# Kernel optimization log

Hardware: AMD Instinct MI355X
Metric: run time of the kernel (lower is better)

Reference implementation:

```python
import jax, jax.numpy as jnp
import numpy as np
from jax import lax

ENC_DIM, DEC_DIM, ATT_DIM, CONV_CH, KSIZE, ATT_ODIM = 1024, 1024, 512, 32, 50, 1024
SCALING = 2.0


def setup_inputs() -> dict:
    key = jax.random.key(0)
    ks = jax.random.split(key, 12)
    B, T = 32, 2000
    enc_pad = jax.random.normal(ks[0], (B, T, ENC_DIM), dtype=jnp.float32)
    enc_len = jax.random.randint(ks[1], (B,), 1000, T + 1, dtype=jnp.int32)
    dec_h = jax.random.normal(ks[2], (B, 1, DEC_DIM), dtype=jnp.float32)
    att_prev = jax.random.uniform(ks[3], (B, T), dtype=jnp.float32)
    s = 0.02
    W_enc = jax.random.normal(ks[4], (ENC_DIM, ATT_DIM), dtype=jnp.float32) * s
    b_enc = jnp.zeros((ATT_DIM,), jnp.float32)
    W_dec = jax.random.normal(ks[5], (DEC_DIM, ATT_DIM), dtype=jnp.float32) * s
    b_dec = jnp.zeros((ATT_DIM,), jnp.float32)
    W_att = jax.random.normal(ks[6], (CONV_CH, ATT_DIM), dtype=jnp.float32) * s
    b_att = jnp.zeros((ATT_DIM,), jnp.float32)
    # Conv2d(1, C, kernel=(1, 2K+1)) acting on (B,1,1,T) == 1D conv kernel (C,1,2K+1)
    conv_w = jax.random.normal(ks[7], (CONV_CH, 1, 2 * KSIZE + 1), dtype=jnp.float32) * s
    gvec = jax.random.normal(ks[8], (ATT_DIM, 1), dtype=jnp.float32) * s
    W_o = jax.random.normal(ks[9], (ENC_DIM, ATT_ODIM), dtype=jnp.float32) * s
    b_o = jnp.zeros((ATT_ODIM,), jnp.float32)
    return {"enc_pad": enc_pad, "enc_len": enc_len, "dec_h": dec_h, "att_prev": att_prev,
            "W_enc": W_enc, "b_enc": b_enc, "W_dec": W_dec, "b_dec": b_dec,
            "W_att": W_att, "b_att": b_att, "conv_w": conv_w, "gvec": gvec,
            "W_o": W_o, "b_o": b_o}


def reference(enc_pad, enc_len, dec_h, att_prev, W_enc, b_enc, W_dec, b_dec,
              W_att, b_att, conv_w, gvec, W_o, b_o):
    B, T, _ = enc_pad.shape
    enc_h = enc_pad @ W_enc + b_enc                           # [B,T,A]
    # location conv: (B,1,T) * (C,1,K) -> (B,C,T), SAME padding
    att_conv = lax.conv_general_dilated(
        att_prev[:, None, :], conv_w, window_strides=(1,),
        padding=[(KSIZE, KSIZE)], dimension_numbers=("NCH", "OIH", "NCH"))
    att_conv = jnp.transpose(att_conv, (0, 2, 1)) @ W_att + b_att  # [B,T,A]
    dec_term = (dec_h.reshape(B, DEC_DIM) @ W_dec + b_dec)[:, None, :]  # [B,1,A]
    att_state = jnp.tanh(enc_h + dec_term + att_conv)         # [B,T,A]
    e = (att_state @ gvec)[:, :, 0]                           # [B,T]
    mask = jnp.arange(T)[None, :] >= enc_len[:, None]         # True = padded
    e = jnp.where(mask, jnp.float32(-1e15), e)
    attn = jax.nn.softmax(SCALING * e, axis=1)                # [B,T]
    c = jnp.einsum("bt,btd->bd", attn, enc_pad)               # [B,enc_dim]
    c = c @ W_o + b_o                                         # [B,att_odim]
    return c, attn
```

## Files before the change

kernel.cpp:

```cpp
#include <hip/hip_runtime.h>
#include <stdint.h>
#include <stddef.h>

#define T_LEN   2000
#define BATCH   32
#define ROWS    64000
#define KDIM    1024
#define ADIM    512
#define CCH     32
#define KW      101
#define PADA    40

typedef _Float16 half8_t  __attribute__((ext_vector_type(8)));
typedef float    float4_t __attribute__((ext_vector_type(4)));

__device__ __forceinline__ half8_t pack8(float4_t a, float4_t b) {
    half8_t r;
    r[0] = (_Float16)a.x; r[1] = (_Float16)a.y;
    r[2] = (_Float16)a.z; r[3] = (_Float16)a.w;
    r[4] = (_Float16)b.x; r[5] = (_Float16)b.y;
    r[6] = (_Float16)b.z; r[7] = (_Float16)b.w;
    return r;
}

__device__ __forceinline__ float tanh_fast(float x) {
    float ax = __builtin_fabsf(x);
    ax = fminf(ax, 15.f);
    float e = __expf(2.f * ax);
    float t = 1.f - 2.f / (e + 1.f);
    return (x < 0.f) ? -t : t;
}

__device__ __forceinline__ void glds16(const void* g, void* l) {
    __builtin_amdgcn_global_load_lds((const __attribute__((address_space(1))) uint32_t*)g,
                                     (__attribute__((address_space(3))) uint32_t*)l,
                                     16, 0, 0);
}

#define OFF_WENCT 0
#define OFF_WATTT 1048576
#define OFF_CONVA 1081344
#define OFF_DTERM 5177344
#define OFF_EPART 5242880
#define OFF_CPART 5498880

__global__ __launch_bounds__(256) void k_prep_we(const float* __restrict__ We,
                                                 _Float16* __restrict__ Wet) {
    __shared__ float tile[32][33];
    const int k0 = blockIdx.x * 32, n0 = blockIdx.y * 32;
    const int tx = threadIdx.x & 31, ty = threadIdx.x >> 5;
#pragma unroll
    for (int i = 0; i < 4; ++i)
        tile[ty + i * 8][tx] = We[(size_t)(k0 + ty + i * 8) * ADIM + n0 + tx];
    __syncthreads();
#pragma unroll
    for (int i = 0; i < 4; ++i)
        Wet[(size_t)(n0 + ty + i * 8) * KDIM + k0 + tx] = (_Float16)tile[tx][ty + i * 8];
}

__global__ __launch_bounds__(512) void k_prep_wat(const float* __restrict__ Wa,
                                                  _Float16* __restrict__ Wat) {
    const int n = threadIdx.x;
#pragma unroll
    for (int c = 0; c < CCH; ++c)
        Wat[n * CCH + c] = (_Float16)Wa[c * ADIM + n];
}

__global__ __launch_bounds__(256) void k_dterm(const float* __restrict__ dec_h,
                                               const float* __restrict__ W_dec,
                                               const float* __restrict__ be,
                                               const float* __restrict__ bd,
                                               const float* __restrict__ ba,
                                               float* __restrict__ dterm) {
    __shared__ float dh[KDIM];
    __shared__ float part[256];
    const int b = blockIdx.x, a0 = blockIdx.y * 128, tid = threadIdx.x;
#pragma unroll
    for (int i = 0; i < 4; ++i) dh[tid + i * 256] = dec_h[b * KDIM + tid + i * 256];
    __syncthreads();
    const int a = a0 + (tid & 127), kh = (tid >> 7) * 512;
    float s = 0.f;
#pragma unroll 8
    for (int k = 0; k < 512; ++k) s += dh[kh + k] * W_dec[(size_t)(kh + k) * ADIM + a];
    part[tid] = s;
    __syncthreads();
    if (tid < 128) {
        const int aa = a0 + tid;
        dterm[b * ADIM + aa] = part[tid] + part[tid + 128] + be[aa] + bd[aa] + ba[aa];
    }
}

__global__ __launch_bounds__(256) void k_conv(const float* __restrict__ att_prev,
                                              const float* __restrict__ conv_w,
                                              _Float16* __restrict__ convA) {
    __shared__ float ap[128 + 100];
    __shared__ float w[CCH * KW];
    int b = blockIdx.y, tt = blockIdx.x;
    int t0 = tt * 128;
    for (int i = threadIdx.x; i < 228; i += 256) {
        int t = t0 - 50 + i;
        ap[i] = (t >= 0 && t < T_LEN) ? att_prev[b * T_LEN + t] : 0.f;
    }
    for (int i = threadIdx.x; i < CCH * KW; i += 256) w[i] = conv_w[i];
    __syncthreads();
    for (int idx = threadIdx.x; idx < 128 * CCH; idx += 256) {
        int tl = idx >> 5, c = idx & 31;
        int t = t0 + tl;
        if (t < T_LEN) {
            float s = 0.f;
#pragma unroll
            for (int j = 0; j < KW; ++j) s += ap[tl + j] * w[c * KW + j];
            convA[(size_t)(b * T_LEN + t) * CCH + c] = (_Float16)s;
        }
    }
}

__global__ __launch_bounds__(512, 1) void k_gemm_e(const float* __restrict__ enc,
                                                   const _Float16* __restrict__ Wet,
                                                   const _Float16* __restrict__ convA,
                                                   const _Float16* __restrict__ Wat,
                                                   const float* __restrict__ dterm,
                                                   const float* __restrict__ gvec,
                                                   float* __restrict__ epart) {
    __shared__ __attribute__((aligned(16))) _Float16 Ah[128 * PADA];
    __shared__ __attribute__((aligned(16))) _Float16 Bh[512 * 32];

    const int tid  = threadIdx.x;
    const int m0   = blockIdx.x * 128;
    const int wave = tid >> 6, lane = tid & 63;
    const int quad = lane >> 4, c16 = lane & 15;
    const int wm = (wave >> 2) * 64, wn = (wave & 3) * 128;

    float4_t acc[4][8];
#pragma unroll
    for (int i = 0; i < 4; ++i)
#pragma unroll
        for (int j = 0; j < 8; ++j) acc[i][j] = (float4_t){0.f, 0.f, 0.f, 0.f};

    const int arow = tid >> 2, aseg = tid & 3;
    const float* aBase = enc + (size_t)(m0 + arow) * KDIM + aseg * 8;
    const int bl4 = lane >> 2, bseg = lane & 3;

    float4_t pa0 = ((const float4_t*)aBase)[0];
    float4_t pa1 = ((const float4_t*)aBase)[1];

    for (int kk = 0; kk < 32; ++kk) {
        const int k0 = kk * 32;
        __syncthreads();
        *(half8_t*)&Ah[arow * PADA + aseg * 8] = pack8(pa0, pa1);
#pragma unroll
        for (int p = 0; p < 4; ++p) {
            const int nb = wave * 64 + p * 16 + bl4;
            glds16(Wet + (size_t)nb * KDIM + k0 + bseg * 8, &Bh[nb * 32 + bseg * 8]);
        }
        __syncthreads();
        {
            const int kn = (kk < 31) ? (k0 + 32) : k0;
            pa0 = ((const float4_t*)(aBase + kn))[0];
            pa1 = ((const float4_t*)(aBase + kn))[1];
        }
        half8_t af[4], bf[8];
#pragma unroll
        for (int i = 0; i < 4; ++i)
            af[i] = *(const half8_t*)&Ah[(wm + i * 16 + c16) * PADA + quad * 8];
#pragma unroll
        for (int j = 0; j < 8; ++j)
            bf[j] = *(const half8_t*)&Bh[(wn + j * 16 + c16) * 32 + quad * 8];
#pragma unroll
        for (int i = 0; i < 4; ++i)
#pragma unroll
            for (int j = 0; j < 8; ++j)
                acc[i][j] = __builtin_amdgcn_mfma_f32_16x16x32_f16(af[i], bf[j], acc[i][j], 0, 0, 0);
    }

    __syncthreads();
    *(half8_t*)&Ah[arow * PADA + aseg * 8] =
        *(const half8_t*)(convA + (size_t)(m0 + arow) * CCH + aseg * 8);
    {
        const half8_t* bs = (const half8_t*)(Wat + tid * CCH);
#pragma unroll
        for (int s4 = 0; s4 < 4; ++s4) *(half8_t*)&Bh[tid * 32 + s4 * 8] = bs[s4];
    }
    __syncthreads();
    {
        half8_t af[4], bf[8];
#pragma unroll
        for (int i = 0; i < 4; ++i)
            af[i] = *(const half8_t*)&Ah[(wm + i * 16 + c16) * PADA + quad * 8];
#pragma unroll
        for (int j = 0; j < 8; ++j)
            bf[j] = *(const half8_t*)&Bh[(wn + j * 16 + c16) * 32 + quad * 8];
#pragma unroll
        for (int i = 0; i < 4; ++i)
#pragma unroll
            for (int j = 0; j < 8; ++j)
                acc[i][j] = __builtin_amdgcn_mfma_f32_16x16x32_f16(af[i], bf[j], acc[i][j], 0, 0, 0);
    }

    __syncthreads();
    float* e_lds = (float*)Ah;
#pragma unroll
    for (int i = 0; i < 4; ++i) {
        const int rl0 = wm + i * 16 + quad * 4;
#pragma unroll
        for (int r = 0; r < 4; ++r) {
            const int grow = m0 + rl0 + r;
            const int b = grow / T_LEN;
            float s = 0.f;
#pragma unroll
            for (int j = 0; j < 8; ++j) {
                const int col = wn + j * 16 + c16;
                const float v = acc[i][j][r] + dterm[b * ADIM + col];
                s += tanh_fast(v) * gvec[col];
            }
#pragma unroll
            for (int off = 1; off < 16; off <<= 1) s += __shfl_xor(s, off);
            if (c16 == 0) e_lds[(rl0 + r) * 4 + (wave & 3)] = s;
        }
    }
    __syncthreads();
    if (tid < 128) {
        float4_t q = ((const float4_t*)e_lds)[tid];
        epart[m0 + tid] = q.x + q.y + q.z + q.w;
    }
}

__global__ __launch_bounds__(512) void k_softmax(const float* __restrict__ epart,
                                                 const int* __restrict__ enc_len,
                                                 float* __restrict__ attn) {
    __shared__ float ex[T_LEN];
    __shared__ float red[8];
    const int b = blockIdx.x, tid = threadIdx.x;
    const int len = enc_len[b];
    float lmax = -3.4e38f;
    for (int t = tid; t < T_LEN; t += 512) {
        float lg = (t < len) ? 2.f * epart[b * T_LEN + t] : -2e15f;
        ex[t] = lg;
        lmax = fmaxf(lmax, lg);
    }
    for (int off = 1; off < 64; off <<= 1) lmax = fmaxf(lmax, __shfl_xor(lmax, off));
    if ((tid & 63) == 0) red[tid >> 6] = lmax;
    __syncthreads();
    const float m = fmaxf(fmaxf(fmaxf(red[0], red[1]), fmaxf(red[2], red[3])),
                          fmaxf(fmaxf(red[4], red[5]), fmaxf(red[6], red[7])));
    float lsum = 0.f;
    for (int t = tid; t < T_LEN; t += 512) {
        float p = __expf(ex[t] - m);
        ex[t] = p;
        lsum += p;
    }
    for (int off = 1; off < 64; off <<= 1) lsum += __shfl_xor(lsum, off);
    __syncthreads();
    if ((tid & 63) == 0) red[tid >> 6] = lsum;
    __syncthreads();
    const float inv = 1.f / (red[0] + red[1] + red[2] + red[3] + red[4] + red[5] + red[6] + red[7]);
    for (int t = tid; t < T_LEN; t += 512) attn[b * T_LEN + t] = ex[t] * inv;
}

__global__ __launch_bounds__(256) void k_cpart(const float* __restrict__ attn,
                                               const float* __restrict__ enc,
                                               float* __restrict__ cpart) {
    const int b = blockIdx.y, tc = blockIdx.x, tid = threadIdx.x;
    const int t0 = tc * 125;
    float4_t s = (float4_t){0.f, 0.f, 0.f, 0.f};
    const float4_t* ep = (const float4_t*)(enc + (size_t)b * T_LEN * KDIM) + tid;
    const float* ap = attn + b * T_LEN + t0;
#pragma unroll 5
    for (int tt = 0; tt < 125; ++tt) {
        const float w = ap[tt];
        float4_t v = ep[(size_t)(t0 + tt) * 256];
        s += v * w;
    }
    *(float4_t*)&cpart[(size_t)(tc * BATCH + b) * KDIM + tid * 4] = s;
}

__global__ __launch_bounds__(256) void k_out(const float* __restrict__ cpart,
                                             const float* __restrict__ W_o,
                                             const float* __restrict__ b_o,
                                             float* __restrict__ out_c) {
    __shared__ float cm[KDIM];
    const int b = blockIdx.x, tid = threadIdx.x;
    for (int d = tid; d < KDIM; d += 256) {
        float s = 0.f;
#pragma unroll
        for (int p = 0; p < 16; ++p) s += cpart[(size_t)(p * BATCH + b) * KDIM + d];
        cm[d] = s;
    }
    __syncthreads();
    const int o = blockIdx.y * 256 + tid;
    float s = b_o[o];
#pragma unroll 8
    for (int d = 0; d < KDIM; ++d) s += cm[d] * W_o[(size_t)d * KDIM + o];
    out_c[b * KDIM + o] = s;
}

extern "C" void kernel_launch(void* const* d_in, const int* in_sizes, int n_in,
                              void* d_out, int out_size, void* d_ws, size_t ws_size,
                              hipStream_t stream) {
    const float* enc      = (const float*)d_in[0];
    const int*   enc_len  = (const int*)d_in[1];
    const float* dec_h    = (const float*)d_in[2];
    const float* att_prev = (const float*)d_in[3];
    const float* W_enc    = (const float*)d_in[4];
    const float* b_enc    = (const float*)d_in[5];
    const float* W_dec    = (const float*)d_in[6];
    const float* b_dec    = (const float*)d_in[7];
    const float* W_att    = (const float*)d_in[8];
    const float* b_att    = (const float*)d_in[9];
    const float* conv_w   = (const float*)d_in[10];
    const float* gvec     = (const float*)d_in[11];
    const float* W_o      = (const float*)d_in[12];
    const float* b_o      = (const float*)d_in[13];

    float* out_c    = (float*)d_out;
    float* out_attn = out_c + BATCH * KDIM;

    char* ws = (char*)d_ws;
    _Float16* Wet   = (_Float16*)(ws + OFF_WENCT);
    _Float16* Wat   = (_Float16*)(ws + OFF_WATTT);
    _Float16* convA = (_Float16*)(ws + OFF_CONVA);
    float*    dterm = (float*)(ws + OFF_DTERM);
    float*    epart = (float*)(ws + OFF_EPART);
    float*    cpart = (float*)(ws + OFF_CPART);

    k_prep_we<<<dim3(32, 16), 256, 0, stream>>>(W_enc, Wet);
    k_prep_wat<<<1, 512, 0, stream>>>(W_att, Wat);
    k_dterm<<<dim3(BATCH, 4), 256, 0, stream>>>(dec_h, W_dec, b_enc, b_dec, b_att, dterm);
    k_conv<<<dim3(16, BATCH), 256, 0, stream>>>(att_prev, conv_w, convA);
    k_gemm_e<<<500, 512, 0, stream>>>(enc, Wet, convA, Wat, dterm, gvec, epart);
    k_softmax<<<BATCH, 512, 0, stream>>>(epart, enc_len, out_attn);
    k_cpart<<<dim3(16, BATCH), 256, 0, stream>>>(out_attn, enc, cpart);
    k_out<<<dim3(BATCH, 4), 256, 0, stream>>>(cpart, W_o, b_o, out_c);
}
```

Baseline: 628.0 us.

## Merge prep kernels, halve GEMM tile rows, swizzle B LDS, hoist epilogue loads

Four preparation kernels are merged into one launch that dispatches on block index, removing three launches. The main GEMM now uses 64-row tiles with 256 threads and 1000 blocks, so occupancy and CU coverage go up but the same B tile is reloaded twice as often. B rows in LDS get an XOR swizzle to cut bank conflicts. The epilogue hoists gvec and dterm into registers, since a 64-row tile can span at most two batches, and tanh uses a hardware reciprocal.

```diff
diff --git a/kernel.cpp b/kernel.cpp
--- a/kernel.cpp
+++ b/kernel.cpp
@@ -27,7 +27,7 @@
     float ax = __builtin_fabsf(x);
     ax = fminf(ax, 15.f);
     float e = __expf(2.f * ax);
-    float t = 1.f - 2.f / (e + 1.f);
+    float t = 1.f - 2.f * __builtin_amdgcn_rcpf(e + 1.f);
     return (x < 0.f) ? -t : t;
 }
 
@@ -44,92 +44,97 @@
 #define OFF_EPART 5242880
 #define OFF_CPART 5498880
 
-__global__ __launch_bounds__(256) void k_prep_we(const float* __restrict__ We,
-                                                 _Float16* __restrict__ Wet) {
-    __shared__ float tile[32][33];
-    const int k0 = blockIdx.x * 32, n0 = blockIdx.y * 32;
-    const int tx = threadIdx.x & 31, ty = threadIdx.x >> 5;
-#pragma unroll
-    for (int i = 0; i < 4; ++i)
-        tile[ty + i * 8][tx] = We[(size_t)(k0 + ty + i * 8) * ADIM + n0 + tx];
-    __syncthreads();
-#pragma unroll
-    for (int i = 0; i < 4; ++i)
-        Wet[(size_t)(n0 + ty + i * 8) * KDIM + k0 + tx] = (_Float16)tile[tx][ty + i * 8];
-}
-
-__global__ __launch_bounds__(512) void k_prep_wat(const float* __restrict__ Wa,
-                                                  _Float16* __restrict__ Wat) {
-    const int n = threadIdx.x;
-#pragma unroll
-    for (int c = 0; c < CCH; ++c)
-        Wat[n * CCH + c] = (_Float16)Wa[c * ADIM + n];
-}
-
-__global__ __launch_bounds__(256) void k_dterm(const float* __restrict__ dec_h,
-                                               const float* __restrict__ W_dec,
-                                               const float* __restrict__ be,
-                                               const float* __restrict__ bd,
-                                               const float* __restrict__ ba,
-                                               float* __restrict__ dterm) {
-    __shared__ float dh[KDIM];
-    __shared__ float part[256];
-    const int b = blockIdx.x, a0 = blockIdx.y * 128, tid = threadIdx.x;
-#pragma unroll
-    for (int i = 0; i < 4; ++i) dh[tid + i * 256] = dec_h[b * KDIM + tid + i * 256];
-    __syncthreads();
-    const int a = a0 + (tid & 127), kh = (tid >> 7) * 512;
-    float s = 0.f;
+__global__ __launch_bounds__(256) void k_prep(const float* __restrict__ We,
+                                              const float* __restrict__ Wa,
+                                              const float* __restrict__ dec_h,
+                                              const float* __restrict__ W_dec,
+                                              const float* __restrict__ be,
+                                              const float* __restrict__ bd,
+                                              const float* __restrict__ ba,
+                                              const float* __restrict__ att_prev,
+                                              const float* __restrict__ conv_w,
+                                              _Float16* __restrict__ Wet,
+                                              _Float16* __restrict__ Wat,
+                                              float* __restrict__ dterm,
+                                              _Float16* __restrict__ convA) {
+    __shared__ float smem[3460];
+    const int blk = blockIdx.x, tid = threadIdx.x;
+
+    if (blk < 512) {
+        float (*tile)[33] = (float(*)[33])smem;
+        const int k0 = (blk >> 4) * 32, n0 = (blk & 15) * 32;
+        const int tx = tid & 31, ty = tid >> 5;
+#pragma unroll
+        for (int i = 0; i < 4; ++i)
+            tile[ty + i * 8][tx] = We[(size_t)(k0 + ty + i * 8) * ADIM + n0 + tx];
+        __syncthreads();
+#pragma unroll
+        for (int i = 0; i < 4; ++i)
+            Wet[(size_t)(n0 + ty + i * 8) * KDIM + k0 + tx] = (_Float16)tile[tx][ty + i * 8];
+    } else if (blk < 640) {
+        float* dh = smem;
+        float* part = smem + 1024;
+        const int idx = blk - 512, b = idx >> 2, a0 = (idx & 3) * 128;
+#pragma unroll
+        for (int i = 0; i < 4; ++i) dh[tid + i * 256] = dec_h[b * KDIM + tid + i * 256];
+        __syncthreads();
+        const int a = a0 + (tid & 127), kh = (tid >> 7) * 512;
+        float s = 0.f;
 #pragma unroll 8
-    for (int k = 0; k < 512; ++k) s += dh[kh + k] * W_dec[(size_t)(kh + k) * ADIM + a];
-    part[tid] = s;
-    __syncthreads();
-    if (tid < 128) {
-        const int aa = a0 + tid;
-        dterm[b * ADIM + aa] = part[tid] + part[tid + 128] + be[aa] + bd[aa] + ba[aa];
-    }
-}
-
-__global__ __launch_bounds__(256) void k_conv(const float* __restrict__ att_prev,
-                                              const float* __restrict__ conv_w,
-                                              _Float16* __restrict__ convA) {
-    __shared__ float ap[128 + 100];
-    __shared__ float w[CCH * KW];
-    int b = blockIdx.y, tt = blockIdx.x;
-    int t0 = tt * 128;
-    for (int i = threadIdx.x; i < 228; i += 256) {
-        int t = t0 - 50 + i;
-        ap[i] = (t >= 0 && t < T_LEN) ? att_prev[b * T_LEN + t] : 0.f;
-    }
-    for (int i = threadIdx.x; i < CCH * KW; i += 256) w[i] = conv_w[i];
-    __syncthreads();
-    for (int idx = threadIdx.x; idx < 128 * CCH; idx += 256) {
-        int tl = idx >> 5, c = idx & 31;
-        int t = t0 + tl;
-        if (t < T_LEN) {
-            float s = 0.f;
-#pragma unroll
-            for (int j = 0; j < KW; ++j) s += ap[tl + j] * w[c * KW + j];
-            convA[(size_t)(b * T_LEN + t) * CCH + c] = (_Float16)s;
-        }
-    }
-}
-
-__global__ __launch_bounds__(512, 1) void k_gemm_e(const float* __restrict__ enc,
-                                                   const _Float16* __restrict__ Wet,
-                                                   const _Float16* __restrict__ convA,
-                                                   const _Float16* __restrict__ Wat,
-                                                   const float* __restrict__ dterm,
-                                                   const float* __restrict__ gvec,
-                                                   float* __restrict__ epart) {
-    __shared__ __attribute__((aligned(16))) _Float16 Ah[128 * PADA];
+        for (int k = 0; k < 512; ++k) s += dh[kh + k] * W_dec[(size_t)(kh + k) * ADIM + a];
+        part[tid] = s;
+        __syncthreads();
+        if (tid < 128) {
+            const int aa = a0 + tid;
+            dterm[b * ADIM + aa] = part[tid] + part[tid + 128] + be[aa] + bd[aa] + ba[aa];
+        }
+    } else if (blk < 1152) {
+        float* ap = smem;
+        float* w  = smem + 228;
+        const int idx = blk - 640, b = idx >> 4, tt = idx & 15;
+        const int t0 = tt * 128;
+        for (int i = tid; i < 228; i += 256) {
+            int t = t0 - 50 + i;
+            ap[i] = (t >= 0 && t < T_LEN) ? att_prev[b * T_LEN + t] : 0.f;
+        }
+        for (int i = tid; i < CCH * KW; i += 256) w[i] = conv_w[i];
+        __syncthreads();
+        for (int idx2 = tid; idx2 < 128 * CCH; idx2 += 256) {
+            int tl = idx2 >> 5, c = idx2 & 31;
+            int t = t0 + tl;
+            if (t < T_LEN) {
+                float s = 0.f;
+#pragma unroll
+                for (int j = 0; j < KW; ++j) s += ap[tl + j] * w[c * KW + j];
+                convA[(size_t)(b * T_LEN + t) * CCH + c] = (_Float16)s;
+            }
+        }
+    } else {
+#pragma unroll
+        for (int rr = 0; rr < 2; ++rr) {
+            const int n = tid * 2 + rr;
+#pragma unroll
+            for (int c = 0; c < CCH; ++c)
+                Wat[n * CCH + c] = (_Float16)Wa[c * ADIM + n];
+        }
+    }
+}
+
+__global__ __launch_bounds__(256) void k_gemm_e(const float* __restrict__ enc,
+                                                const _Float16* __restrict__ Wet,
+                                                const _Float16* __restrict__ convA,
+                                                const _Float16* __restrict__ Wat,
+                                                const float* __restrict__ dterm,
+                                                const float* __restrict__ gvec,
+                                                float* __restrict__ epart) {
+    __shared__ __attribute__((aligned(16))) _Float16 Ah[64 * PADA];
     __shared__ __attribute__((aligned(16))) _Float16 Bh[512 * 32];
 
     const int tid  = threadIdx.x;
-    const int m0   = blockIdx.x * 128;
+    const int m0   = blockIdx.x * 64;
     const int wave = tid >> 6, lane = tid & 63;
     const int quad = lane >> 4, c16 = lane & 15;
-    const int wm = (wave >> 2) * 64, wn = (wave & 3) * 128;
+    const int wn = wave * 128;
 
     float4_t acc[4][8];
 #pragma unroll
@@ -139,7 +144,7 @@
 
     const int arow = tid >> 2, aseg = tid & 3;
     const float* aBase = enc + (size_t)(m0 + arow) * KDIM + aseg * 8;
-    const int bl4 = lane >> 2, bseg = lane & 3;
+    const int rowl = lane >> 2, segst = lane & 3;
 
     float4_t pa0 = ((const float4_t*)aBase)[0];
     float4_t pa1 = ((const float4_t*)aBase)[1];
@@ -149,9 +154,10 @@
         __syncthreads();
         *(half8_t*)&Ah[arow * PADA + aseg * 8] = pack8(pa0, pa1);
 #pragma unroll
-        for (int p = 0; p < 4; ++p) {
-            const int nb = wave * 64 + p * 16 + bl4;
-            glds16(Wet + (size_t)nb * KDIM + k0 + bseg * 8, &Bh[nb * 32 + bseg * 8]);
+        for (int p = 0; p < 8; ++p) {
+            const int nb = wn + p * 16 + rowl;
+            const int segsrc = segst ^ ((nb >> 1) & 3);
+            glds16(Wet + (size_t)nb * KDIM + k0 + segsrc * 8, &Bh[(wn + p * 16) * 32]);
         }
         __syncthreads();
         {
@@ -162,10 +168,13 @@
         half8_t af[4], bf[8];
 #pragma unroll
         for (int i = 0; i < 4; ++i)
-            af[i] = *(const half8_t*)&Ah[(wm + i * 16 + c16) * PADA + quad * 8];
-#pragma unroll
-        for (int j = 0; j < 8; ++j)
-            bf[j] = *(const half8_t*)&Bh[(wn + j * 16 + c16) * 32 + quad * 8];
+            af[i] = *(const half8_t*)&Ah[(i * 16 + c16) * PADA + quad * 8];
+#pragma unroll
+        for (int j = 0; j < 8; ++j) {
+            const int r = wn + j * 16 + c16;
+            const int sb = quad ^ ((r >> 1) & 3);
+            bf[j] = *(const half8_t*)&Bh[r * 32 + sb * 8];
+        }
 #pragma unroll
         for (int i = 0; i < 4; ++i)
 #pragma unroll
@@ -176,20 +185,26 @@
     __syncthreads();
     *(half8_t*)&Ah[arow * PADA + aseg * 8] =
         *(const half8_t*)(convA + (size_t)(m0 + arow) * CCH + aseg * 8);
-    {
-        const half8_t* bs = (const half8_t*)(Wat + tid * CCH);
-#pragma unroll
-        for (int s4 = 0; s4 < 4; ++s4) *(half8_t*)&Bh[tid * 32 + s4 * 8] = bs[s4];
+#pragma unroll
+    for (int rr = 0; rr < 2; ++rr) {
+        const int n = tid * 2 + rr;
+        const int sw = (n >> 1) & 3;
+#pragma unroll
+        for (int s = 0; s < 4; ++s)
+            *(half8_t*)&Bh[n * 32 + s * 8] = *(const half8_t*)(Wat + n * CCH + (s ^ sw) * 8);
     }
     __syncthreads();
     {
         half8_t af[4], bf[8];
 #pragma unroll
         for (int i = 0; i < 4; ++i)
-            af[i] = *(const half8_t*)&Ah[(wm + i * 16 + c16) * PADA + quad * 8];
-#pragma unroll
-        for (int j = 0; j < 8; ++j)
-            bf[j] = *(const half8_t*)&Bh[(wn + j * 16 + c16) * 32 + quad * 8];
+            af[i] = *(const half8_t*)&Ah[(i * 16 + c16) * PADA + quad * 8];
+#pragma unroll
+        for (int j = 0; j < 8; ++j) {
+            const int r = wn + j * 16 + c16;
+            const int sb = quad ^ ((r >> 1) & 3);
+            bf[j] = *(const half8_t*)&Bh[r * 32 + sb * 8];
+        }
 #pragma unroll
         for (int i = 0; i < 4; ++i)
 #pragma unroll
@@ -197,29 +212,37 @@
                 acc[i][j] = __builtin_amdgcn_mfma_f32_16x16x32_f16(af[i], bf[j], acc[i][j], 0, 0, 0);
     }
 
+    float g[8], dt0[8], dt1[8];
+    const int b0 = m0 / T_LEN, bt = (m0 + 63) / T_LEN;
+    const int lim = (b0 + 1) * T_LEN;
+#pragma unroll
+    for (int j = 0; j < 8; ++j) {
+        const int col = wn + j * 16 + c16;
+        g[j]   = gvec[col];
+        dt0[j] = dterm[b0 * ADIM + col];
+        dt1[j] = dterm[bt * ADIM + col];
+    }
     __syncthreads();
     float* e_lds = (float*)Ah;
 #pragma unroll
     for (int i = 0; i < 4; ++i) {
-        const int rl0 = wm + i * 16 + quad * 4;
 #pragma unroll
         for (int r = 0; r < 4; ++r) {
-            const int grow = m0 + rl0 + r;
-            const int b = grow / T_LEN;
+            const int rl = i * 16 + quad * 4 + r;
+            const bool hi = (m0 + rl) >= lim;
             float s = 0.f;
 #pragma unroll
             for (int j = 0; j < 8; ++j) {
-                const int col = wn + j * 16 + c16;
-                const float v = acc[i][j][r] + dterm[b * ADIM + col];
-                s += tanh_fast(v) * gvec[col];
+                const float dv = hi ? dt1[j] : dt0[j];
+                s += tanh_fast(acc[i][j][r] + dv) * g[j];
             }
 #pragma unroll
             for (int off = 1; off < 16; off <<= 1) s += __shfl_xor(s, off);
-            if (c16 == 0) e_lds[(rl0 + r) * 4 + (wave & 3)] = s;
-        }
-    }
-    __syncthreads();
-    if (tid < 128) {
+            if (c16 == 0) e_lds[rl * 4 + wave] = s;
+        }
+    }
+    __syncthreads();
+    if (tid < 64) {
         float4_t q = ((const float4_t*)e_lds)[tid];
         epart[m0 + tid] = q.x + q.y + q.z + q.w;
     }
@@ -323,11 +346,9 @@
     float*    epart = (float*)(ws + OFF_EPART);
     float*    cpart = (float*)(ws + OFF_CPART);
 
-    k_prep_we<<<dim3(32, 16), 256, 0, stream>>>(W_enc, Wet);
-    k_prep_wat<<<1, 512, 0, stream>>>(W_att, Wat);
-    k_dterm<<<dim3(BATCH, 4), 256, 0, stream>>>(dec_h, W_dec, b_enc, b_dec, b_att, dterm);
-    k_conv<<<dim3(16, BATCH), 256, 0, stream>>>(att_prev, conv_w, convA);
-    k_gemm_e<<<500, 512, 0, stream>>>(enc, Wet, convA, Wat, dterm, gvec, epart);
+    k_prep<<<1153, 256, 0, stream>>>(W_enc, W_att, dec_h, W_dec, b_enc, b_dec, b_att,
+                                     att_prev, conv_w, Wet, Wat, dterm, convA);
+    k_gemm_e<<<1000, 256, 0, stream>>>(enc, Wet, convA, Wat, dterm, gvec, epart);
     k_softmax<<<BATCH, 512, 0, stream>>>(epart, enc_len, out_attn);
     k_cpart<<<dim3(16, BATCH), 256, 0, stream>>>(out_attn, enc, cpart);
     k_out<<<dim3(BATCH, 4), 256, 0, stream>>>(cpart, W_o, b_o, out_c);
```

Result: slower. 662.2 us (+5.4%).
